# Performance work log

Hardware: AMD Instinct MI355X
Metric: run time of the kernel (lower is better)

The kernel has to match this reference:

```python
import jax, jax.numpy as jnp
import numpy as np

K, D, BETA = 512, 64, 0.25


def conv(x, w, b, s, p):
    # x: NCHW, w: OIHW (torch Conv2d layout)
    y = jax.lax.conv_general_dilated(x, w, (s, s), [(p, p), (p, p)],
                                     dimension_numbers=('NCHW', 'OIHW', 'NCHW'))
    if b is not None:
        y = y + b[None, :, None, None]
    return y


def conv_t(x, w, b, s, p):
    # torch ConvTranspose2d: w is (Cin, Cout, k, k). Equivalent to a dilated conv
    # with flipped, transposed kernel and padding k-1-p.
    k = w.shape[2]
    w2 = jnp.transpose(jnp.flip(w, (2, 3)), (1, 0, 2, 3))  # -> (Cout, Cin, k, k)
    y = jax.lax.conv_general_dilated(x, w2, (1, 1), [(k - 1 - p, k - 1 - p)] * 2,
                                     lhs_dilation=(s, s),
                                     dimension_numbers=('NCHW', 'OIHW', 'NCHW'))
    return y + b[None, :, None, None]


def res_stack(x, w1s, w2s):
    # w1s: (n_blocks, C_mid, C_in, 3, 3); w2s: (n_blocks, C_in, C_mid, 1, 1); no bias
    for i in range(w1s.shape[0]):
        h = conv(jax.nn.relu(x), w1s[i], None, 1, 1)
        h = conv(jax.nn.relu(h), w2s[i], None, 1, 0)
        x = x + h
    return jax.nn.relu(x)


def setup_inputs() -> dict:
    key = jax.random.key(0)
    ks = jax.random.split(key, 24)
    rn = lambda k, shape, s=0.05: (jax.random.normal(k, shape, jnp.float32) * s)
    return {
        'x': jax.random.normal(ks[0], (64, 3, 128, 128), jnp.float32),
        'enc_w1': rn(ks[1], (64, 3, 4, 4)),    'enc_b1': rn(ks[2], (64,)),
        'enc_w2': rn(ks[3], (128, 64, 4, 4)),  'enc_b2': rn(ks[4], (128,)),
        'enc_w3': rn(ks[5], (128, 128, 3, 3)), 'enc_b3': rn(ks[6], (128,)),
        'enc_w4': rn(ks[7], (128, 128, 3, 3)), 'enc_b4': rn(ks[8], (128,)),
        'enc_res_w1': rn(ks[9], (2, 64, 128, 3, 3)),
        'enc_res_w2': rn(ks[10], (2, 128, 64, 1, 1)),
        'enc_adj_w': rn(ks[11], (64, 128, 1, 1)), 'enc_adj_b': rn(ks[12], (64,)),
        'E': jax.random.uniform(ks[13], (K, D), jnp.float32, -1.0 / K, 1.0 / K),
        'dec_adj_w': rn(ks[14], (128, 64, 3, 3)), 'dec_adj_b': rn(ks[15], (128,)),
        'dec_res_w1': rn(ks[16], (2, 64, 128, 3, 3)),
        'dec_res_w2': rn(ks[17], (2, 128, 64, 1, 1)),
        'tc1_w': rn(ks[18], (128, 64, 4, 4)), 'tc1_b': rn(ks[19], (64,)),
        'tc2_w': rn(ks[20], (64, 3, 4, 4)),  'tc2_b': rn(ks[21], (3,)),
    }


def vq_vae_forward(x, enc_w1, enc_b1, enc_w2, enc_b2, enc_w3, enc_b3, enc_w4, enc_b4,
                   enc_res_w1, enc_res_w2, enc_adj_w, enc_adj_b, E,
                   dec_adj_w, dec_adj_b, dec_res_w1, dec_res_w2, tc1_w, tc1_b, tc2_w, tc2_b):
    relu = jax.nn.relu
    # ---- Encoder ----
    h = relu(conv(x, enc_w1, enc_b1, 2, 1))      # (B,64,64,64)
    h = relu(conv(h, enc_w2, enc_b2, 2, 1))      # (B,128,32,32)
    h = relu(conv(h, enc_w3, enc_b3, 1, 1))
    h = conv(h, enc_w4, enc_b4, 1, 1)
    h = res_stack(h, enc_res_w1, enc_res_w2)
    Ze = conv(h, enc_adj_w, enc_adj_b, 1, 0)     # (B,D,32,32)
    # ---- Vector quantizer (eval mode, use_EMA=False) ----
    Zt = jnp.transpose(Ze, (0, 2, 3, 1))          # (B,H,W,D)
    flat = Zt.reshape(-1, D)                      # (N,D), N=65536
    dist = (jnp.sum(flat ** 2, axis=1, keepdims=True)
            + jnp.sum(E ** 2, axis=1)
            - 2.0 * flat @ E.T)                    # (N,K)
    idx = jnp.argmin(dist, axis=1)                # (N,)
    Zq = E[idx].reshape(Zt.shape)
    e_latent_loss = jnp.mean((jax.lax.stop_gradient(Zq) - Zt) ** 2)
    q_latent_loss = jnp.mean((Zq - jax.lax.stop_gradient(Zt)) ** 2)
    e_and_q = q_latent_loss + BETA * e_latent_loss
    Zq_st = Zt + jax.lax.stop_gradient(Zq - Zt)   # straight-through
    Zq_nchw = jnp.transpose(Zq_st, (0, 3, 1, 2))
    counts = jnp.zeros((K,), jnp.float32).at[idx].add(1.0)
    probs = counts / jnp.sum(counts)
    entropy_bits = -jnp.sum(probs * jnp.log2(probs + 1e-10))  # zero-count terms vanish
    est_words = 2.0 ** entropy_bits
    # ---- Decoder ----
    g = conv(Zq_nchw, dec_adj_w, dec_adj_b, 1, 1)  # (B,128,32,32)
    g = res_stack(g, dec_res_w1, dec_res_w2)
    g = relu(conv_t(g, tc1_w, tc1_b, 2, 1))        # (B,64,64,64)
    x_recon = conv_t(g, tc2_w, tc2_b, 2, 1)        # (B,3,128,128)
    return e_and_q, x_recon, e_latent_loss, q_latent_loss, est_words


def reference(x, enc_w1, enc_b1, enc_w2, enc_b2, enc_w3, enc_b3, enc_w4, enc_b4,
              enc_res_w1, enc_res_w2, enc_adj_w, enc_adj_b, E,
              dec_adj_w, dec_adj_b, dec_res_w1, dec_res_w2, tc1_w, tc1_b, tc2_w, tc2_b):
    return vq_vae_forward(x, enc_w1, enc_b1, enc_w2, enc_b2, enc_w3, enc_b3, enc_w4, enc_b4,
                          enc_res_w1, enc_res_w2, enc_adj_w, enc_adj_b, E,
                          dec_adj_w, dec_adj_b, dec_res_w1, dec_res_w2, tc1_w, tc1_b, tc2_w, tc2_b)
```

## Files before the change

### kernel.cpp

```cpp
#include <hip/hip_runtime.h>
#include <math.h>


typedef unsigned short u16;
typedef __attribute__((ext_vector_type(8))) short bf16x8;
typedef __attribute__((ext_vector_type(4))) float f32x4;

__device__ __forceinline__ float bf2f(u16 h) {
    union { unsigned u; float f; } v; v.u = ((unsigned)h) << 16; return v.f;
}
__device__ __forceinline__ u16 f2bf(float f) {
    union { float f; unsigned u; } v; v.f = f;
    unsigned r = v.u + 0x7FFFu + ((v.u >> 16) & 1u);
    return (u16)(r >> 16);
}
__device__ __forceinline__ unsigned relu2(unsigned x) {
    return x & ~(((x & 0x80008000u) >> 15) * 0xFFFFu);
}

struct Taps { int s; int ntaps; int dh[16]; int dw[16]; };

template<int CIN, int COUT, bool RELU_IN, bool RELU_OUT, bool HAS_BIAS, bool RESID>
__global__ __launch_bounds__(256)
void mfma_conv_k(const u16* __restrict__ in, const u16* __restrict__ wT,
                 const float* __restrict__ bias, u16* __restrict__ out,
                 int Hin, int Win, int Hout, int Wout, int OS, int OPH, int OPW,
                 Taps taps)
{
    constexpr int TM = 2, TN = 4;
    constexpr int LDA = 40;
    constexpr int NCH = CIN / 32;

    __shared__ alignas(16) u16 aT[128 * LDA];
    __shared__ alignas(16) u16 bT[64 * LDA];

    const int tid = threadIdx.x;
    const int m0 = blockIdx.x * 128;
    const int colbase = blockIdx.y << 6;
    const int n_img = m0 >> 10;
    const int pixbase = m0 & 1023;

    const int r = tid >> 1, half = tid & 1;
    const int pr = pixbase + r;
    const int ohr = pr >> 5, owr = pr & 31;
    const u16* inb = in + (size_t)n_img * Hin * Win * CIN;

    const int wv = tid >> 6, lane = tid & 63;
    const int q = lane >> 4, l16 = lane & 15;
    const int mbase = wv * 32;
    const bool bload = r < 64;

    f32x4 acc[TM][TN] = {};

    const int total_it = taps.ntaps * NCH;
    uint4 pa0, pa1, pb0 = {0,0,0,0}, pb1 = {0,0,0,0};

#define LOAD_IT(IT) do {                                                        \
        int t_ = (IT) / NCH, cc_ = ((IT) % NCH) * 32;                           \
        int ih_ = ohr * taps.s + taps.dh[t_];                                   \
        int iw_ = owr * taps.s + taps.dw[t_];                                   \
        bool ok_ = ((unsigned)ih_ < (unsigned)Hin) &&                           \
                   ((unsigned)iw_ < (unsigned)Win);                             \
        pa0 = (uint4){0,0,0,0}; pa1 = (uint4){0,0,0,0};                         \
        if (ok_) {                                                              \
            const u16* as_ = inb + ((size_t)ih_ * Win + iw_) * CIN              \
                             + half * 16 + cc_;                                 \
            pa0 = *(const uint4*)(as_);                                         \
            pa1 = *(const uint4*)(as_ + 8);                                     \
        }                                                                       \
        if (bload) {                                                            \
            const u16* bs_ = wT + ((size_t)t_ * COUT + colbase + r) * CIN       \
                             + half * 16 + cc_;                                 \
            pb0 = *(const uint4*)(bs_);                                         \
            pb1 = *(const uint4*)(bs_ + 8);                                     \
        }                                                                       \
    } while (0)

    LOAD_IT(0);

    for (int it = 0; it < total_it; ++it) {
        __syncthreads();
        uint4 a0 = pa0, a1 = pa1;
        if (RELU_IN) {
            a0.x = relu2(a0.x); a0.y = relu2(a0.y); a0.z = relu2(a0.z); a0.w = relu2(a0.w);
            a1.x = relu2(a1.x); a1.y = relu2(a1.y); a1.z = relu2(a1.z); a1.w = relu2(a1.w);
        }
        *(uint4*)&aT[r * LDA + half * 16]     = a0;
        *(uint4*)&aT[r * LDA + half * 16 + 8] = a1;
        if (bload) {
            *(uint4*)&bT[r * LDA + half * 16]     = pb0;
            *(uint4*)&bT[r * LDA + half * 16 + 8] = pb1;
        }
        __syncthreads();
        if (it + 1 < total_it) LOAD_IT(it + 1);

        bf16x8 afr[TM], bfr[TN];
        #pragma unroll
        for (int tm = 0; tm < TM; ++tm)
            afr[tm] = *(const bf16x8*)&aT[(mbase + tm*16 + l16) * LDA + q * 8];
        #pragma unroll
        for (int tn = 0; tn < TN; ++tn)
            bfr[tn] = *(const bf16x8*)&bT[(tn*16 + l16) * LDA + q * 8];
        #pragma unroll
        for (int tm = 0; tm < TM; ++tm)
            #pragma unroll
            for (int tn = 0; tn < TN; ++tn)
                acc[tm][tn] = __builtin_amdgcn_mfma_f32_16x16x32_bf16(
                    afr[tm], bfr[tn], acc[tm][tn], 0, 0, 0);
    }
#undef LOAD_IT

    #pragma unroll
    for (int tm = 0; tm < TM; ++tm) {
        #pragma unroll
        for (int tn = 0; tn < TN; ++tn) {
            const int col = colbase + tn*16 + l16;
            const float bv = HAS_BIAS ? bias[col] : 0.0f;
            #pragma unroll
            for (int rg = 0; rg < 4; ++rg) {
                const int m = mbase + tm*16 + q*4 + rg;
                const int pix = pixbase + m;
                const int oh = pix >> 5, ow = pix & 31;
                size_t oidx = (((size_t)n_img * Hout + (oh*OS + OPH)) * Wout
                               + (ow*OS + OPW)) * COUT + col;
                float v = acc[tm][tn][rg] + bv;
                if (RESID) v += bf2f(out[oidx]);
                if (RELU_OUT) v = fmaxf(v, 0.0f);
                out[oidx] = f2bf(v);
            }
        }
    }
}

__global__ __launch_bounds__(256)
void conv1_mfma_k(const float* __restrict__ x, const u16* __restrict__ wc1b,
                  const float* __restrict__ b, u16* __restrict__ out)
{
    __shared__ alignas(16) u16 smem[15360];
    u16* aT0 = smem;
    u16* aT1 = smem + 5120;
    u16* bT0 = smem + 10240;
    u16* bT1 = smem + 12800;

    const int tid = threadIdx.x;
    const int gbase = blockIdx.x * 128;
    const int r = tid >> 1, half = tid & 1;
    const int p = gbase + r;
    const int ow = p & 63, oh = (p >> 6) & 63, n = p >> 12;
    const float* xb = x + (size_t)n * 3 * 16384;

    {
        int row = tid >> 2, sub = tid & 3;
        *(uint4*)&bT0[row*40 + sub*8] = *(const uint4*)(wc1b + row*64 + sub*8);
        *(uint4*)&bT1[row*40 + sub*8] = *(const uint4*)(wc1b + row*64 + 32 + sub*8);
    }

    float vals[24];
    const int kb = half * 24;
    #pragma unroll
    for (int j = 0; j < 24; ++j) {
        int k = kb + j;
        int ci = k >> 4, kh = (k >> 2) & 3, kw = k & 3;
        int ih = oh*2 - 1 + kh, iw = ow*2 - 1 + kw;
        bool ok = ((unsigned)ih < 128u) && ((unsigned)iw < 128u);
        vals[j] = ok ? xb[ci*16384 + ih*128 + iw] : 0.0f;
    }
    unsigned pk[12];
    #pragma unroll
    for (int jj = 0; jj < 12; ++jj)
        pk[jj] = (unsigned)f2bf(vals[2*jj]) | ((unsigned)f2bf(vals[2*jj+1]) << 16);
    unsigned* a0row = (unsigned*)&aT0[r * 40];
    unsigned* a1row = (unsigned*)&aT1[r * 40];
    if (half == 0) {
        #pragma unroll
        for (int jj = 0; jj < 12; ++jj) a0row[jj] = pk[jj];
    } else {
        a0row[12] = pk[0]; a0row[13] = pk[1];
        a0row[14] = pk[2]; a0row[15] = pk[3];
        #pragma unroll
        for (int jj = 4; jj < 12; ++jj) a1row[jj - 4] = pk[jj];
        *(uint4*)&aT1[r*40 + 16] = (uint4){0,0,0,0};
        *(uint4*)&aT1[r*40 + 24] = (uint4){0,0,0,0};
    }
    __syncthreads();

    const int wv = tid >> 6, lane = tid & 63;
    const int q = lane >> 4, l16 = lane & 15;
    const int mbase = wv * 32;

    f32x4 acc[2][4] = {};
    bf16x8 af0[2], af1[2], bf0[4], bf1[4];
    #pragma unroll
    for (int tm = 0; tm < 2; ++tm) {
        af0[tm] = *(const bf16x8*)&aT0[(mbase + tm*16 + l16) * 40 + q * 8];
        af1[tm] = *(const bf16x8*)&aT1[(mbase + tm*16 + l16) * 40 + q * 8];
    }
    #pragma unroll
    for (int tn = 0; tn < 4; ++tn) {
        bf0[tn] = *(const bf16x8*)&bT0[(tn*16 + l16) * 40 + q * 8];
        bf1[tn] = *(const bf16x8*)&bT1[(tn*16 + l16) * 40 + q * 8];
    }
    #pragma unroll
    for (int tm = 0; tm < 2; ++tm)
        #pragma unroll
        for (int tn = 0; tn < 4; ++tn) {
            acc[tm][tn] = __builtin_amdgcn_mfma_f32_16x16x32_bf16(
                af0[tm], bf0[tn], acc[tm][tn], 0, 0, 0);
            acc[tm][tn] = __builtin_amdgcn_mfma_f32_16x16x32_bf16(
                af1[tm], bf1[tn], acc[tm][tn], 0, 0, 0);
        }

    float bv[4];
    #pragma unroll
    for (int tn = 0; tn < 4; ++tn) bv[tn] = b[tn*16 + l16];

    __syncthreads();
    u16* cbuf = smem;
    #pragma unroll
    for (int tm = 0; tm < 2; ++tm)
        #pragma unroll
        for (int tn = 0; tn < 4; ++tn)
            #pragma unroll
            for (int rg = 0; rg < 4; ++rg) {
                int row = mbase + tm*16 + q*4 + rg;
                int col = tn*16 + l16;
                cbuf[row*72 + col] = f2bf(fmaxf(acc[tm][tn][rg] + bv[tn], 0.0f));
            }
    __syncthreads();

    u16* ob = out + (size_t)gbase * 64;
    #pragma unroll
    for (int it = 0; it < 4; ++it) {
        int j = it * 256 + tid;
        uint4 v = *(const uint4*)&cbuf[(j >> 3) * 72 + (j & 7) * 8];
        *(uint4*)(ob + j * 8) = v;
    }
}

__global__ __launch_bounds__(256)
void tc2_mfma_k(const u16* __restrict__ in, const u16* __restrict__ wT,
                const float* __restrict__ bias, float* __restrict__ out)
{
    constexpr int LDA = 40;
    __shared__ alignas(16) u16 aT[128 * LDA];
    __shared__ alignas(16) u16 bT[16 * LDA];
    __shared__ float cT[128 * 17];

    const int tid = threadIdx.x;
    const int m0 = blockIdx.x * 128;
    const int n_img = m0 >> 12;
    const int pixbase = m0 & 4095;
    const int y0 = pixbase >> 6;

    const int r = tid >> 1, half = tid & 1;
    const int pr = pixbase + r;
    const int yr = pr >> 6, xr = pr & 63;
    const u16* inb = in + (size_t)n_img * 4096 * 64;

    const int wv = tid >> 6, lane = tid & 63;
    const int q = lane >> 4, l16 = lane & 15;
    const int mbase = wv * 32;

    f32x4 acc[2] = {};

    for (int t = 0; t < 9; ++t) {
        const int ih = yr + t/3 - 1;
        const int iw = xr + t%3 - 1;
        const bool ok = ((unsigned)ih < 64u) && ((unsigned)iw < 64u);
        const u16* asrc = ok ? (inb + ((size_t)ih * 64 + iw) * 64 + half * 16) : inb;
        const u16* bsrc = wT + ((size_t)t * 16 + r) * 64 + half * 16;

        for (int c0 = 0; c0 < 64; c0 += 32) {
            __syncthreads();
            uint4 a0 = {0,0,0,0}, a1 = {0,0,0,0};
            if (ok) {
                a0 = *(const uint4*)(asrc + c0);
                a1 = *(const uint4*)(asrc + c0 + 8);
            }
            *(uint4*)&aT[r * LDA + half * 16]     = a0;
            *(uint4*)&aT[r * LDA + half * 16 + 8] = a1;
            if (r < 16) {
                *(uint4*)&bT[r * LDA + half * 16]     = *(const uint4*)(bsrc + c0);
                *(uint4*)&bT[r * LDA + half * 16 + 8] = *(const uint4*)(bsrc + c0 + 8);
            }
            __syncthreads();

            bf16x8 af0 = *(const bf16x8*)&aT[(mbase + l16) * LDA + q * 8];
            bf16x8 af1 = *(const bf16x8*)&aT[(mbase + 16 + l16) * LDA + q * 8];
            bf16x8 bf  = *(const bf16x8*)&bT[l16 * LDA + q * 8];
            acc[0] = __builtin_amdgcn_mfma_f32_16x16x32_bf16(af0, bf, acc[0], 0, 0, 0);
            acc[1] = __builtin_amdgcn_mfma_f32_16x16x32_bf16(af1, bf, acc[1], 0, 0, 0);
        }
    }

    #pragma unroll
    for (int tm = 0; tm < 2; ++tm)
        #pragma unroll
        for (int rg = 0; rg < 4; ++rg)
            cT[(mbase + tm*16 + q*4 + rg) * 17 + l16] = acc[tm][rg];
    __syncthreads();

    #pragma unroll
    for (int it = 0; it < 6; ++it) {
        int j = it * 256 + tid;
        int co  = j >> 9;
        int rem = j & 511;
        int ohl = rem >> 7;
        int ow  = rem & 127;
        int oh  = 2*y0 + ohl;
        int lp  = (ohl >> 1) * 64 + (ow >> 1);
        int col = ((ohl & 1) * 2 + (ow & 1)) * 4 + co;
        float v = cT[lp * 17 + col] + bias[co];
        out[(((size_t)n_img * 3 + co) * 128 + oh) * 128 + ow] = v;
    }
}

__global__ __launch_bounds__(256)
void vq_mfma_k(const u16* __restrict__ Ze, const u16* __restrict__ Ebf,
               const float* __restrict__ enorm1, u16* __restrict__ Zq,
               u16* __restrict__ idx_out, float* __restrict__ sse)
{
    __shared__ alignas(16) u16 eld[256 * 72];
    __shared__ float en1s[256];
    __shared__ int bestk_s[128];
    __shared__ float red[256];

    const int tid = threadIdx.x;
    const int lane = tid & 63, wv = tid >> 6;
    const int q = lane >> 4, l16 = lane & 15;
    const int pb = blockIdx.x * 128 + wv * 32;

    bf16x8 alo[2], ahi[2];
    #pragma unroll
    for (int tile = 0; tile < 2; ++tile) {
        const u16* zp = Ze + (size_t)(pb + tile*16 + l16) * 64;
        alo[tile] = *(const bf16x8*)(zp + q * 8);
        ahi[tile] = *(const bf16x8*)(zp + 32 + q * 8);
    }

    unsigned key[2][4] = {{0xFFFFFFFFu,0xFFFFFFFFu,0xFFFFFFFFu,0xFFFFFFFFu},
                          {0xFFFFFFFFu,0xFFFFFFFFu,0xFFFFFFFFu,0xFFFFFFFFu}};

    for (int k0 = 0; k0 < 512; k0 += 256) {
        __syncthreads();
        const uint4* src = (const uint4*)(Ebf + k0 * 64);
        #pragma unroll
        for (int i = tid; i < 2048; i += 256) {
            int row = i >> 3, sub = i & 7;
            *(uint4*)&eld[row * 72 + sub * 8] = src[i];
        }
        en1s[tid] = enorm1[k0 + tid];
        __syncthreads();

        for (int t = 0; t < 16; ++t) {
            const int nl = t * 16 + l16;
            bf16x8 b0 = *(const bf16x8*)&eld[nl * 72 + q * 8];
            bf16x8 b1 = *(const bf16x8*)&eld[nl * 72 + 32 + q * 8];
            const float en1 = en1s[nl];
            const unsigned ng = (unsigned)(k0 + nl);
            #pragma unroll
            for (int tile = 0; tile < 2; ++tile) {
                f32x4 acc = {0.0f, 0.0f, 0.0f, 0.0f};
                acc = __builtin_amdgcn_mfma_f32_16x16x32_bf16(alo[tile], b0, acc, 0, 0, 0);
                acc = __builtin_amdgcn_mfma_f32_16x16x32_bf16(ahi[tile], b1, acc, 0, 0, 0);
                #pragma unroll
                for (int rg = 0; rg < 4; ++rg) {
                    float sc = fmaf(acc[rg], -2.0f, en1);
                    unsigned kk2 = (__float_as_uint(sc) & 0xFFFFFE00u) | ng;
                    key[tile][rg] = min(key[tile][rg], kk2);
                }
            }
        }
    }

    #pragma unroll
    for (int m = 1; m < 16; m <<= 1) {
        #pragma unroll
        for (int tile = 0; tile < 2; ++tile)
            #pragma unroll
            for (int rg = 0; rg < 4; ++rg) {
                unsigned o = (unsigned)__shfl_xor((int)key[tile][rg], m, 64);
                key[tile][rg] = min(key[tile][rg], o);
            }
    }
    if (l16 == 0) {
        #pragma unroll
        for (int tile = 0; tile < 2; ++tile)
            #pragma unroll
            for (int rg = 0; rg < 4; ++rg)
                bestk_s[wv * 32 + tile * 16 + q * 4 + rg] = (int)(key[tile][rg] & 511u);
    }
    __syncthreads();

    const int pos = tid >> 1, seg = tid & 1;
    const int p = blockIdx.x * 128 + pos;
    const int k = bestk_s[pos];
    const u16* ep = Ebf + (size_t)k * 64 + seg * 32;
    const u16* zp = Ze + (size_t)p * 64 + seg * 32;
    u16* qp = Zq + (size_t)p * 64 + seg * 32;
    float local = 0.0f;
    #pragma unroll
    for (int h = 0; h < 4; ++h) {
        uint4 ev = *(const uint4*)(ep + h * 8);
        uint4 zv = *(const uint4*)(zp + h * 8);
        *(uint4*)(qp + h * 8) = ev;
        unsigned ea[4] = {ev.x, ev.y, ev.z, ev.w};
        unsigned za[4] = {zv.x, zv.y, zv.z, zv.w};
        #pragma unroll
        for (int j = 0; j < 4; ++j) {
            float d0 = bf2f((u16)(ea[j] & 0xFFFFu)) - bf2f((u16)(za[j] & 0xFFFFu));
            float d1 = bf2f((u16)(ea[j] >> 16))     - bf2f((u16)(za[j] >> 16));
            local = fmaf(d0, d0, fmaf(d1, d1, local));
        }
    }
    if (seg == 0) idx_out[p] = (u16)k;
    red[tid] = local;
    __syncthreads();
    for (int s = 128; s > 0; s >>= 1) {
        if (tid < s) red[tid] += red[tid + s];
        __syncthreads();
    }
    if (tid == 0) atomicAdd(sse, red[0]);
}

__global__ __launch_bounds__(256)
void hist_k(const u16* __restrict__ idx, float* __restrict__ counts)
{
    __shared__ int red[256];
    const int k = blockIdx.x;
    const int tid = threadIdx.x;
    int c = 0;
    const uint4* p4 = (const uint4*)idx;
    for (int i = tid; i < 8192; i += 256) {
        uint4 v = p4[i];
        unsigned ua[4] = {v.x, v.y, v.z, v.w};
        #pragma unroll
        for (int j = 0; j < 4; ++j) {
            c += ((ua[j] & 0xFFFFu) == (unsigned)k);
            c += ((ua[j] >> 16)     == (unsigned)k);
        }
    }
    red[tid] = c;
    __syncthreads();
    for (int s = 128; s > 0; s >>= 1) {
        if (tid < s) red[tid] += red[tid + s];
        __syncthreads();
    }
    if (tid == 0) counts[k] = (float)red[0];
}

__device__ __forceinline__ void wconv_tf(const float* __restrict__ w,
                                         u16* __restrict__ o,
                                         int COUT, int CIN, int KK, int i)
{
    int ci = i % CIN; int t = i / CIN; int co = t % COUT; t /= COUT;
    o[i] = f2bf(w[(co*CIN + ci)*KK + t]);
}

__global__ __launch_bounds__(256)
void prep_k(const float* __restrict__ enc_w1, const float* __restrict__ enc_w2,
            const float* __restrict__ enc_w3, const float* __restrict__ enc_w4,
            const float* __restrict__ enc_res_w1, const float* __restrict__ enc_res_w2,
            const float* __restrict__ dec_res_w1, const float* __restrict__ dec_res_w2,
            const float* __restrict__ enc_adj_w, const float* __restrict__ dec_adj_w,
            const float* __restrict__ tc1_w, const float* __restrict__ tc2_w,
            const float* __restrict__ E,
            u16* __restrict__ wc1b, u16* __restrict__ wc2, u16* __restrict__ wc3,
            u16* __restrict__ wc4, u16* __restrict__ wer1, u16* __restrict__ wer2,
            u16* __restrict__ wdr1, u16* __restrict__ wdr2, u16* __restrict__ weadj,
            u16* __restrict__ wdadj, u16* __restrict__ wtc1, u16* __restrict__ wtc2b,
            u16* __restrict__ Ebf, float* __restrict__ enorm1, float* __restrict__ sse)
{
    const int b = blockIdx.x, tid = threadIdx.x;
    if (b < 512) {
        wconv_tf(enc_w2, wc2, 128, 64, 16, b * 256 + tid);
    } else if (b < 1088) {
        wconv_tf(enc_w3, wc3, 128, 128, 9, (b - 512) * 256 + tid);
    } else if (b < 1664) {
        wconv_tf(enc_w4, wc4, 128, 128, 9, (b - 1088) * 256 + tid);
    } else if (b < 2240) {
        int i = (b - 1664) * 256 + tid;
        int sub = i / 73728, rem = i - sub * 73728;
        wconv_tf(enc_res_w1 + sub * 73728, wer1 + sub * 73728, 64, 128, 9, rem);
    } else if (b < 2816) {
        int i = (b - 2240) * 256 + tid;
        int sub = i / 73728, rem = i - sub * 73728;
        wconv_tf(dec_res_w1 + sub * 73728, wdr1 + sub * 73728, 64, 128, 9, rem);
    } else if (b < 2880) {
        int i = (b - 2816) * 256 + tid;
        int sub = i >> 13, rem = i & 8191;
        wconv_tf(enc_res_w2 + sub * 8192, wer2 + sub * 8192, 128, 64, 1, rem);
    } else if (b < 2944) {
        int i = (b - 2880) * 256 + tid;
        int sub = i >> 13, rem = i & 8191;
        wconv_tf(dec_res_w2 + sub * 8192, wdr2 + sub * 8192, 128, 64, 1, rem);
    } else if (b < 2976) {
        wconv_tf(enc_adj_w, weadj, 64, 128, 1, (b - 2944) * 256 + tid);
    } else if (b < 3264) {
        wconv_tf(dec_adj_w, wdadj, 128, 64, 9, (b - 2976) * 256 + tid);
    } else if (b < 3776) {
        int i = (b - 3264) * 256 + tid;
        int ci = i & 127; int co = (i >> 7) & 63; int t = (i >> 13) & 3; int p = i >> 15;
        int poh = p >> 1, pw = p & 1; int a = t >> 1, bb = t & 1;
        int kh = poh ? (a ? 2 : 0) : (a ? 3 : 1);
        int kw = pw  ? (bb ? 2 : 0) : (bb ? 3 : 1);
        wtc1[i] = f2bf(tc1_w[((ci*64 + co)*4 + kh)*4 + kw]);
    } else if (b < 3812) {
        int i = (b - 3776) * 256 + tid;
        int ci = i & 63; int col = (i >> 6) & 15; int t = i >> 10;
        int dh = t / 3 - 1, dw = t % 3 - 1;
        int pp = col >> 2, co = col & 3;
        float v = 0.0f;
        if (co < 3) {
            int poh = pp >> 1, pw = pp & 1;
            int kh = poh ? (dh == 1 ? 0 : (dh == 0 ? 2 : -1))
                         : (dh == 0 ? 1 : (dh == -1 ? 3 : -1));
            int kw = pw  ? (dw == 1 ? 0 : (dw == 0 ? 2 : -1))
                         : (dw == 0 ? 1 : (dw == -1 ? 3 : -1));
            if (kh >= 0 && kw >= 0)
                v = tc2_w[((ci*3 + co)*4 + kh)*4 + kw];
        }
        wtc2b[i] = f2bf(v);
    } else if (b < 3814) {
        int k = (b - 3812) * 256 + tid;
        float s = 0.0f;
        #pragma unroll
        for (int d = 0; d < 64; ++d) {
            u16 h = f2bf(E[k*64 + d]);
            Ebf[k*64 + d] = h;
            float v = bf2f(h);
            s = fmaf(v, v, s);
        }
        enorm1[k] = s + 1.0f;
    } else if (b < 3830) {
        int i = (b - 3814) * 256 + tid;
        int co = i >> 6, k = i & 63;
        float v = 0.0f;
        if (k < 48) {
            int ci = k >> 4, kh = (k >> 2) & 3, kw = k & 3;
            v = enc_w1[((co*3 + ci)*4 + kh)*4 + kw];
        }
        wc1b[i] = f2bf(v);
    } else {
        if (tid == 0) sse[0] = 0.0f;
    }
}

__global__ void finalize_k(const float* __restrict__ counts, const float* __restrict__ sse,
                           float* __restrict__ out_head, float* __restrict__ out_tail)
{
    __shared__ float red[512];
    int t = threadIdx.x;
    float pr = counts[t] / 65536.0f;
    red[t] = -pr * log2f(pr + 1e-10f);
    __syncthreads();
    for (int s = 256; s > 0; s >>= 1) {
        if (t < s) red[t] += red[t + s];
        __syncthreads();
    }
    if (t == 0) {
        float entropy = red[0];
        float mse = sse[0] / 4194304.0f;
        out_head[0] = 1.25f * mse;
        out_tail[0] = mse;
        out_tail[1] = mse;
        out_tail[2] = exp2f(entropy);
    }
}

extern "C" void kernel_launch(void* const* d_in, const int* in_sizes, int n_in,
                              void* d_out, int out_size, void* d_ws, size_t ws_size,
                              hipStream_t stream)
{
    const float* x         = (const float*)d_in[0];
    const float* enc_w1    = (const float*)d_in[1];
    const float* enc_b1    = (const float*)d_in[2];
    const float* enc_w2    = (const float*)d_in[3];
    const float* enc_b2    = (const float*)d_in[4];
    const float* enc_w3    = (const float*)d_in[5];
    const float* enc_b3    = (const float*)d_in[6];
    const float* enc_w4    = (const float*)d_in[7];
    const float* enc_b4    = (const float*)d_in[8];
    const float* enc_res_w1= (const float*)d_in[9];
    const float* enc_res_w2= (const float*)d_in[10];
    const float* enc_adj_w = (const float*)d_in[11];
    const float* enc_adj_b = (const float*)d_in[12];
    const float* Ecb       = (const float*)d_in[13];
    const float* dec_adj_w = (const float*)d_in[14];
    const float* dec_adj_b = (const float*)d_in[15];
    const float* dec_res_w1= (const float*)d_in[16];
    const float* dec_res_w2= (const float*)d_in[17];
    const float* tc1_w     = (const float*)d_in[18];
    const float* tc1_b     = (const float*)d_in[19];
    const float* tc2_w     = (const float*)d_in[20];
    const float* tc2_b     = (const float*)d_in[21];

    char* wsb = (char*)d_ws;
    u16*   wc2   = (u16*)(wsb + 0);
    u16*   wc3   = (u16*)(wsb + 262144);
    u16*   wc4   = (u16*)(wsb + 557056);
    u16*   wer1  = (u16*)(wsb + 851968);
    u16*   wer2  = (u16*)(wsb + 1146880);
    u16*   weadj = (u16*)(wsb + 1179648);
    u16*   wdadj = (u16*)(wsb + 1196032);
    u16*   wdr1  = (u16*)(wsb + 1343488);
    u16*   wdr2  = (u16*)(wsb + 1638400);
    u16*   wtc1  = (u16*)(wsb + 1671168);
    u16*   wtc2b = (u16*)(wsb + 1933312);
    float* counts= (float*)(wsb + 1951744);
    float* sse   = counts + 512;
    u16*   Ebf   = (u16*)(wsb + 1955840);
    float* enorm1= (float*)(wsb + 2021376);
    u16*   wc1b  = (u16*)(wsb + 2023424);
    u16*   H1    = (u16*)(wsb + 2097152);
    u16*   TR    = (u16*)(wsb + 35651584);
    u16*   H3    = (u16*)(wsb + 52428800);
    u16*   MID   = (u16*)(wsb + 69206016);
    u16*   ZE    = (u16*)(wsb + 77594624);
    u16*   ZQ    = (u16*)(wsb + 85983232);
    u16*   IDX   = (u16*)(wsb + 94371840);
    u16*   TC1O  = H1;

    float* out  = (float*)d_out;
    float* xrec = out + 1;
    float* tail = out + 1 + 3145728;

    Taps t3x3; t3x3.s = 1; t3x3.ntaps = 9;
    for (int kh = 0; kh < 3; ++kh) for (int kw = 0; kw < 3; ++kw) {
        t3x3.dh[kh*3+kw] = kh - 1; t3x3.dw[kh*3+kw] = kw - 1;
    }
    Taps t1x1; t1x1.s = 1; t1x1.ntaps = 1; t1x1.dh[0] = 0; t1x1.dw[0] = 0;
    Taps t4x4; t4x4.s = 2; t4x4.ntaps = 16;
    for (int kh = 0; kh < 4; ++kh) for (int kw = 0; kw < 4; ++kw) {
        t4x4.dh[kh*4+kw] = kh - 1; t4x4.dw[kh*4+kw] = kw - 1;
    }
    const int dtab[2][2] = {{0, -1}, {1, 0}};
    Taps ttc1[4];
    for (int p = 0; p < 4; ++p) {
        ttc1[p].s = 1; ttc1[p].ntaps = 4;
        for (int a = 0; a < 2; ++a) for (int bb = 0; bb < 2; ++bb) {
            ttc1[p].dh[a*2+bb] = dtab[p>>1][a];
            ttc1[p].dw[a*2+bb] = dtab[p&1][bb];
        }
    }

    prep_k<<<3831, 256, 0, stream>>>(enc_w1, enc_w2, enc_w3, enc_w4,
        enc_res_w1, enc_res_w2, dec_res_w1, dec_res_w2, enc_adj_w, dec_adj_w,
        tc1_w, tc2_w, Ecb, wc1b, wc2, wc3, wc4, wer1, wer2, wdr1, wdr2,
        weadj, wdadj, wtc1, wtc2b, Ebf, enorm1, sse);

    conv1_mfma_k<<<2048, 256, 0, stream>>>(x, wc1b, enc_b1, H1);
    mfma_conv_k<64,128,false,true,true,false><<<dim3(512,2), 256, 0, stream>>>
        (H1, wc2, enc_b2, TR, 64, 64, 32, 32, 1, 0, 0, t4x4);
    mfma_conv_k<128,128,false,true,true,false><<<dim3(512,2), 256, 0, stream>>>
        (TR, wc3, enc_b3, H3, 32, 32, 32, 32, 1, 0, 0, t3x3);
    mfma_conv_k<128,128,false,false,true,false><<<dim3(512,2), 256, 0, stream>>>
        (H3, wc4, enc_b4, TR, 32, 32, 32, 32, 1, 0, 0, t3x3);
    for (int i = 0; i < 2; ++i) {
        mfma_conv_k<128,64,true,false,false,false><<<dim3(512,1), 256, 0, stream>>>
            (TR, wer1 + i*73728, nullptr, MID, 32, 32, 32, 32, 1, 0, 0, t3x3);
        mfma_conv_k<64,128,true,false,false,true><<<dim3(512,2), 256, 0, stream>>>
            (MID, wer2 + i*8192, nullptr, TR, 32, 32, 32, 32, 1, 0, 0, t1x1);
    }
    mfma_conv_k<128,64,true,false,true,false><<<dim3(512,1), 256, 0, stream>>>
        (TR, weadj, enc_adj_b, ZE, 32, 32, 32, 32, 1, 0, 0, t1x1);

    vq_mfma_k<<<512, 256, 0, stream>>>(ZE, Ebf, enorm1, ZQ, IDX, sse);
    hist_k<<<512, 256, 0, stream>>>(IDX, counts);

    mfma_conv_k<64,128,false,false,true,false><<<dim3(512,2), 256, 0, stream>>>
        (ZQ, wdadj, dec_adj_b, H3, 32, 32, 32, 32, 1, 0, 0, t3x3);
    for (int i = 0; i < 2; ++i) {
        mfma_conv_k<128,64,true,false,false,false><<<dim3(512,1), 256, 0, stream>>>
            (H3, wdr1 + i*73728, nullptr, MID, 32, 32, 32, 32, 1, 0, 0, t3x3);
        mfma_conv_k<64,128,true,false,false,true><<<dim3(512,2), 256, 0, stream>>>
            (MID, wdr2 + i*8192, nullptr, H3, 32, 32, 32, 32, 1, 0, 0, t1x1);
    }
    for (int p = 0; p < 4; ++p) {
        mfma_conv_k<128,64,true,true,true,false><<<dim3(512,1), 256, 0, stream>>>
            (H3, wtc1 + p*32768, tc1_b, TC1O, 32, 32, 64, 64, 2, p>>1, p&1, ttc1[p]);
    }
    tc2_mfma_k<<<2048, 256, 0, stream>>>(TC1O, wtc2b, tc2_b, xrec);

    finalize_k<<<1, 512, 0, stream>>>(counts, sse, out, tail);
}
```

Before: 524.1 us.

## Fuse residual block convs into one kernel and merge tc1 parity launches

Adds a fused residual-block kernel that computes the 3x3 conv (ReLU in), applies ReLU, keeps the 64-channel intermediate in shared memory, then runs the 1x1 conv plus residual add. Output goes to a ping-pong buffer, so the MID tensor round trip through global memory and half the launches disappear. The four transposed-conv parity launches are also merged into one launch using blockIdx.z to pick taps and weights. In exchange the fused kernel uses more shared memory, which may lower occupancy.

```diff
diff --git a/kernel.cpp b/kernel.cpp
--- a/kernel.cpp
+++ b/kernel.cpp
@@ -20,7 +20,8 @@
 
 struct Taps { int s; int ntaps; int dh[16]; int dw[16]; };
 
-template<int CIN, int COUT, bool RELU_IN, bool RELU_OUT, bool HAS_BIAS, bool RESID>
+template<int CIN, int COUT, bool RELU_IN, bool RELU_OUT, bool HAS_BIAS,
+         bool RESID, bool PAR4>
 __global__ __launch_bounds__(256)
 void mfma_conv_k(const u16* __restrict__ in, const u16* __restrict__ wT,
                  const float* __restrict__ bias, u16* __restrict__ out,
@@ -37,6 +38,11 @@
     const int tid = threadIdx.x;
     const int m0 = blockIdx.x * 128;
     const int colbase = blockIdx.y << 6;
+    const int pz = PAR4 ? blockIdx.z : 0;
+    const int tapo = PAR4 ? pz * 4 : 0;
+    const u16* wTb = PAR4 ? wT + (size_t)pz * 4 * COUT * CIN : wT;
+    const int oph = PAR4 ? (pz >> 1) : OPH;
+    const int opw = PAR4 ? (pz & 1) : OPW;
     const int n_img = m0 >> 10;
     const int pixbase = m0 & 1023;
 
@@ -57,8 +63,8 @@
 
 #define LOAD_IT(IT) do {                                                        \
         int t_ = (IT) / NCH, cc_ = ((IT) % NCH) * 32;                           \
-        int ih_ = ohr * taps.s + taps.dh[t_];                                   \
-        int iw_ = owr * taps.s + taps.dw[t_];                                   \
+        int ih_ = ohr * taps.s + taps.dh[tapo + t_];                            \
+        int iw_ = owr * taps.s + taps.dw[tapo + t_];                            \
         bool ok_ = ((unsigned)ih_ < (unsigned)Hin) &&                           \
                    ((unsigned)iw_ < (unsigned)Win);                             \
         pa0 = (uint4){0,0,0,0}; pa1 = (uint4){0,0,0,0};                         \
@@ -69,7 +75,7 @@
             pa1 = *(const uint4*)(as_ + 8);                                     \
         }                                                                       \
         if (bload) {                                                            \
-            const u16* bs_ = wT + ((size_t)t_ * COUT + colbase + r) * CIN       \
+            const u16* bs_ = wTb + ((size_t)t_ * COUT + colbase + r) * CIN      \
                              + half * 16 + cc_;                                 \
             pb0 = *(const uint4*)(bs_);                                         \
             pb1 = *(const uint4*)(bs_ + 8);                                     \
@@ -121,8 +127,8 @@
                 const int m = mbase + tm*16 + q*4 + rg;
                 const int pix = pixbase + m;
                 const int oh = pix >> 5, ow = pix & 31;
-                size_t oidx = (((size_t)n_img * Hout + (oh*OS + OPH)) * Wout
-                               + (ow*OS + OPW)) * COUT + col;
+                size_t oidx = (((size_t)n_img * Hout + (oh*OS + oph)) * Wout
+                               + (ow*OS + opw)) * COUT + col;
                 float v = acc[tm][tn][rg] + bv;
                 if (RESID) v += bf2f(out[oidx]);
                 if (RELU_OUT) v = fmaxf(v, 0.0f);
@@ -130,6 +136,147 @@
             }
         }
     }
+}
+
+__global__ __launch_bounds__(256)
+void res_fused_k(const u16* __restrict__ in, const u16* __restrict__ w1,
+                 const u16* __restrict__ w2, u16* __restrict__ out)
+{
+    constexpr int LDA = 40;
+    __shared__ alignas(16) u16 smem[20480];
+    u16* aT   = smem;
+    u16* bT   = smem + 5120;
+    u16* mT0  = smem;
+    u16* mT1  = smem + 5120;
+    u16* b2T0 = smem + 10240;
+    u16* b2T1 = smem + 15360;
+
+    const int tid = threadIdx.x;
+    const int m0 = blockIdx.x * 128;
+    const int n_img = m0 >> 10;
+    const int pixbase = m0 & 1023;
+
+    const int r = tid >> 1, half = tid & 1;
+    const int pr = pixbase + r;
+    const int ohr = pr >> 5, owr = pr & 31;
+    const u16* inb = in + (size_t)n_img * 1024 * 128;
+
+    const int wv = tid >> 6, lane = tid & 63;
+    const int q = lane >> 4, l16 = lane & 15;
+    const int mbase = wv * 32;
+    const bool bload = r < 64;
+
+    {
+        const u16* s = w2 + r * 64 + half * 32;
+        u16* d = (half ? b2T1 : b2T0) + r * LDA;
+        *(uint4*)(d)      = *(const uint4*)(s);
+        *(uint4*)(d + 8)  = *(const uint4*)(s + 8);
+        *(uint4*)(d + 16) = *(const uint4*)(s + 16);
+        *(uint4*)(d + 24) = *(const uint4*)(s + 24);
+    }
+
+    f32x4 acc[2][4] = {};
+    uint4 pa0, pa1, pb0 = {0,0,0,0}, pb1 = {0,0,0,0};
+
+#define RLOAD(IT) do {                                                          \
+        int t_ = (IT) >> 2, cc_ = ((IT) & 3) * 32;                              \
+        int ih_ = ohr + t_/3 - 1, iw_ = owr + t_%3 - 1;                         \
+        bool ok_ = ((unsigned)ih_ < 32u) && ((unsigned)iw_ < 32u);              \
+        pa0 = (uint4){0,0,0,0}; pa1 = (uint4){0,0,0,0};                         \
+        if (ok_) {                                                              \
+            const u16* as_ = inb + ((size_t)ih_ * 32 + iw_) * 128               \
+                             + half * 16 + cc_;                                 \
+            pa0 = *(const uint4*)(as_);                                         \
+            pa1 = *(const uint4*)(as_ + 8);                                     \
+        }                                                                       \
+        if (bload) {                                                            \
+            const u16* bs_ = w1 + ((size_t)t_ * 64 + r) * 128                   \
+                             + half * 16 + cc_;                                 \
+            pb0 = *(const uint4*)(bs_);                                         \
+            pb1 = *(const uint4*)(bs_ + 8);                                     \
+        }                                                                       \
+    } while (0)
+
+    RLOAD(0);
+    for (int it = 0; it < 36; ++it) {
+        __syncthreads();
+        uint4 a0 = pa0, a1 = pa1;
+        a0.x = relu2(a0.x); a0.y = relu2(a0.y); a0.z = relu2(a0.z); a0.w = relu2(a0.w);
+        a1.x = relu2(a1.x); a1.y = relu2(a1.y); a1.z = relu2(a1.z); a1.w = relu2(a1.w);
+        *(uint4*)&aT[r * LDA + half * 16]     = a0;
+        *(uint4*)&aT[r * LDA + half * 16 + 8] = a1;
+        if (bload) {
+            *(uint4*)&bT[r * LDA + half * 16]     = pb0;
+            *(uint4*)&bT[r * LDA + half * 16 + 8] = pb1;
+        }
+        __syncthreads();
+        if (it + 1 < 36) RLOAD(it + 1);
+
+        bf16x8 afr[2], bfr[4];
+        #pragma unroll
+        for (int tm = 0; tm < 2; ++tm)
+            afr[tm] = *(const bf16x8*)&aT[(mbase + tm*16 + l16) * LDA + q * 8];
+        #pragma unroll
+        for (int tn = 0; tn < 4; ++tn)
+            bfr[tn] = *(const bf16x8*)&bT[(tn*16 + l16) * LDA + q * 8];
+        #pragma unroll
+        for (int tm = 0; tm < 2; ++tm)
+            #pragma unroll
+            for (int tn = 0; tn < 4; ++tn)
+                acc[tm][tn] = __builtin_amdgcn_mfma_f32_16x16x32_bf16(
+                    afr[tm], bfr[tn], acc[tm][tn], 0, 0, 0);
+    }
+#undef RLOAD
+
+    __syncthreads();
+
+    #pragma unroll
+    for (int tm = 0; tm < 2; ++tm)
+        #pragma unroll
+        for (int tn = 0; tn < 4; ++tn) {
+            u16* dst = (tn < 2) ? mT0 : mT1;
+            const int kc = (tn & 1) * 16 + l16;
+            #pragma unroll
+            for (int rg = 0; rg < 4; ++rg) {
+                int row = mbase + tm*16 + q*4 + rg;
+                dst[row * LDA + kc] = f2bf(fmaxf(acc[tm][tn][rg], 0.0f));
+            }
+        }
+    __syncthreads();
+
+    f32x4 acc2[2][8] = {};
+    #pragma unroll
+    for (int kk = 0; kk < 2; ++kk) {
+        const u16* mp = kk ? mT1 : mT0;
+        const u16* bp = kk ? b2T1 : b2T0;
+        bf16x8 af[2], bf[8];
+        #pragma unroll
+        for (int tm = 0; tm < 2; ++tm)
+            af[tm] = *(const bf16x8*)&mp[(mbase + tm*16 + l16) * LDA + q * 8];
+        #pragma unroll
+        for (int tn = 0; tn < 8; ++tn)
+            bf[tn] = *(const bf16x8*)&bp[(tn*16 + l16) * LDA + q * 8];
+        #pragma unroll
+        for (int tm = 0; tm < 2; ++tm)
+            #pragma unroll
+            for (int tn = 0; tn < 8; ++tn)
+                acc2[tm][tn] = __builtin_amdgcn_mfma_f32_16x16x32_bf16(
+                    af[tm], bf[tn], acc2[tm][tn], 0, 0, 0);
+    }
+
+    #pragma unroll
+    for (int tm = 0; tm < 2; ++tm)
+        #pragma unroll
+        for (int tn = 0; tn < 8; ++tn) {
+            const int col = tn*16 + l16;
+            #pragma unroll
+            for (int rg = 0; rg < 4; ++rg) {
+                const int m = mbase + tm*16 + q*4 + rg;
+                const int pix = pixbase + m;
+                size_t off = ((size_t)n_img * 1024 + pix) * 128 + col;
+                out[off] = f2bf(acc2[tm][tn][rg] + bf2f(in[off]));
+            }
+        }
 }
 
 __global__ __launch_bounds__(256)
@@ -615,7 +762,6 @@
     u16*   H1    = (u16*)(wsb + 2097152);
     u16*   TR    = (u16*)(wsb + 35651584);
     u16*   H3    = (u16*)(wsb + 52428800);
-    u16*   MID   = (u16*)(wsb + 69206016);
     u16*   ZE    = (u16*)(wsb + 77594624);
     u16*   ZQ    = (u16*)(wsb + 85983232);
     u16*   IDX   = (u16*)(wsb + 94371840);
@@ -635,14 +781,12 @@
         t4x4.dh[kh*4+kw] = kh - 1; t4x4.dw[kh*4+kw] = kw - 1;
     }
     const int dtab[2][2] = {{0, -1}, {1, 0}};
-    Taps ttc1[4];
-    for (int p = 0; p < 4; ++p) {
-        ttc1[p].s = 1; ttc1[p].ntaps = 4;
+    Taps ttc1m; ttc1m.s = 1; ttc1m.ntaps = 4;
+    for (int p = 0; p < 4; ++p)
         for (int a = 0; a < 2; ++a) for (int bb = 0; bb < 2; ++bb) {
-            ttc1[p].dh[a*2+bb] = dtab[p>>1][a];
-            ttc1[p].dw[a*2+bb] = dtab[p&1][bb];
-        }
-    }
+            ttc1m.dh[p*4 + a*2 + bb] = dtab[p>>1][a];
+            ttc1m.dw[p*4 + a*2 + bb] = dtab[p&1][bb];
+        }
 
     prep_k<<<3831, 256, 0, stream>>>(enc_w1, enc_w2, enc_w3, enc_w4,
         enc_res_w1, enc_res_w2, dec_res_w1, dec_res_w2, enc_adj_w, dec_adj_w,
@@ -650,36 +794,26 @@
         weadj, wdadj, wtc1, wtc2b, Ebf, enorm1, sse);
 
     conv1_mfma_k<<<2048, 256, 0, stream>>>(x, wc1b, enc_b1, H1);
-    mfma_conv_k<64,128,false,true,true,false><<<dim3(512,2), 256, 0, stream>>>
+    mfma_conv_k<64,128,false,true,true,false,false><<<dim3(512,2), 256, 0, stream>>>
         (H1, wc2, enc_b2, TR, 64, 64, 32, 32, 1, 0, 0, t4x4);
-    mfma_conv_k<128,128,false,true,true,false><<<dim3(512,2), 256, 0, stream>>>
+    mfma_conv_k<128,128,false,true,true,false,false><<<dim3(512,2), 256, 0, stream>>>
         (TR, wc3, enc_b3, H3, 32, 32, 32, 32, 1, 0, 0, t3x3);
-    mfma_conv_k<128,128,false,false,true,false><<<dim3(512,2), 256, 0, stream>>>
+    mfma_conv_k<128,128,false,false,true,false,false><<<dim3(512,2), 256, 0, stream>>>
         (H3, wc4, enc_b4, TR, 32, 32, 32, 32, 1, 0, 0, t3x3);
-    for (int i = 0; i < 2; ++i) {
-        mfma_conv_k<128,64,true,false,false,false><<<dim3(512,1), 256, 0, stream>>>
-            (TR, wer1 + i*73728, nullptr, MID, 32, 32, 32, 32, 1, 0, 0, t3x3);
-        mfma_conv_k<64,128,true,false,false,true><<<dim3(512,2), 256, 0, stream>>>
-            (MID, wer2 + i*8192, nullptr, TR, 32, 32, 32, 32, 1, 0, 0, t1x1);
-    }
-    mfma_conv_k<128,64,true,false,true,false><<<dim3(512,1), 256, 0, stream>>>
+    res_fused_k<<<512, 256, 0, stream>>>(TR, wer1,         wer2,        H3);
+    res_fused_k<<<512, 256, 0, stream>>>(H3, wer1 + 73728, wer2 + 8192, TR);
+    mfma_conv_k<128,64,true,false,true,false,false><<<dim3(512,1), 256, 0, stream>>>
         (TR, weadj, enc_adj_b, ZE, 32, 32, 32, 32, 1, 0, 0, t1x1);
 
     vq_mfma_k<<<512, 256, 0, stream>>>(ZE, Ebf, enorm1, ZQ, IDX, sse);
     hist_k<<<512, 256, 0, stream>>>(IDX, counts);
 
-    mfma_conv_k<64,128,false,false,true,false><<<dim3(512,2), 256, 0, stream>>>
+    mfma_conv_k<64,128,false,false,true,false,false><<<dim3(512,2), 256, 0, stream>>>
         (ZQ, wdadj, dec_adj_b, H3, 32, 32, 32, 32, 1, 0, 0, t3x3);
-    for (int i = 0; i < 2; ++i) {
-        mfma_conv_k<128,64,true,false,false,false><<<dim3(512,1), 256, 0, stream>>>
-            (H3, wdr1 + i*73728, nullptr, MID, 32, 32, 32, 32, 1, 0, 0, t3x3);
-        mfma_conv_k<64,128,true,false,false,true><<<dim3(512,2), 256, 0, stream>>>
-            (MID, wdr2 + i*8192, nullptr, H3, 32, 32, 32, 32, 1, 0, 0, t1x1);
-    }
-    for (int p = 0; p < 4; ++p) {
-        mfma_conv_k<128,64,true,true,true,false><<<dim3(512,1), 256, 0, stream>>>
-            (H3, wtc1 + p*32768, tc1_b, TC1O, 32, 32, 64, 64, 2, p>>1, p&1, ttc1[p]);
-    }
+    res_fused_k<<<512, 256, 0, stream>>>(H3, wdr1,         wdr2,        TR);
+    res_fused_k<<<512, 256, 0, stream>>>(TR, wdr1 + 73728, wdr2 + 8192, H3);
+    mfma_conv_k<128,64,true,true,true,false,true><<<dim3(512,1,4), 256, 0, stream>>>
+        (H3, wtc1, tc1_b, TC1O, 32, 32, 64, 64, 2, 0, 0, ttc1m);
     tc2_mfma_k<<<2048, 256, 0, stream>>>(TC1O, wtc2b, tc2_b, xrec);
 
     finalize_k<<<1, 512, 0, stream>>>(counts, sse, out, tail);
```

Result: faster. 463.5 us (-11.6%).
